# Kernel tuning notes

Hardware: AMD Instinct MI355X
Metric: run time of the kernel (lower is better)

## Reference

```python
import jax, jax.numpy as jnp
import numpy as np

B, D_IN, D_HID, D_OUT = 16384, 256, 512, 256
E, K = 8, 2  # expert_num, activate_num


def setup_inputs() -> dict:
    key = jax.random.key(0)
    ks = jax.random.split(key, 6)
    s_in = 1.0 / np.sqrt(D_IN)
    s_hid = 1.0 / np.sqrt(D_HID)
    return {
        "x": jax.random.normal(ks[0], (B, D_IN), dtype=jnp.float32),
        "Wg": jax.random.normal(ks[1], (D_IN, E), dtype=jnp.float32) * s_in,
        "W1": jax.random.normal(ks[2], (E, D_IN, D_HID), dtype=jnp.float32) * s_in,
        "b1": jnp.zeros((E, D_HID), dtype=jnp.float32),
        "W2": jax.random.normal(ks[3], (E, D_HID, D_OUT), dtype=jnp.float32) * s_hid,
        "b2": jnp.zeros((E, D_OUT), dtype=jnp.float32),
    }


def reference(x, Wg, W1, b1, W2, b2):
    # Gating: logits -> top-k -> softmax over the k selected logits.
    # (nn.Dropout on gate logits is identity at inference.)
    gate_logits = x @ Wg                              # [B, E]
    weights, selected = jax.lax.top_k(gate_logits, K)  # [B, K], [B, K]
    weights = jax.nn.softmax(weights.astype(jnp.float32), axis=1).astype(x.dtype)

    # Expert compute, vectorized over experts (same math as the per-expert
    # gather/compute/scatter loop; tokens not routed to expert e get weight 0).
    h = jax.nn.relu(jnp.einsum("bd,edh->ebh", x, W1) + b1[:, None, :])  # [E, B, H]
    expert_out = jnp.einsum("ebh,eho->ebo", h, W2) + b2[:, None, :]      # [E, B, O]

    # Combine weights: combine[b, e] = sum_k weights[b,k] * [selected[b,k]==e]
    one_hot = jax.nn.one_hot(selected, E, dtype=x.dtype)  # [B, K, E]
    combine = jnp.einsum("bk,bke->be", weights, one_hot)  # [B, E]
    results = jnp.einsum("be,ebo->bo", combine, expert_out)  # [B, O]
    return results
```

## Files before the change

kernel.cpp:

```cpp
#include <hip/hip_runtime.h>
#include <hip/hip_bf16.h>

typedef __bf16 bf16x8 __attribute__((ext_vector_type(8)));
typedef __bf16 bf16x4 __attribute__((ext_vector_type(4)));
typedef float f32x4 __attribute__((ext_vector_type(4)));
typedef float f32x16 __attribute__((ext_vector_type(16)));

#define NTOK 16384
#define DIN  256
#define DHID 512
#define DOUT 256
#define NEXP 8
#define MAXB 264

#define MFMA32(a, b, c) __builtin_amdgcn_mfma_f32_32x32x16_bf16(a, b, c, 0, 0, 0)
#define GLD16(gp, lp)                                                       \
  __builtin_amdgcn_global_load_lds(                                         \
      (__attribute__((address_space(1))) void*)(gp),                        \
      (__attribute__((address_space(3))) void*)(lp), 16, 0, 0)

__global__ __launch_bounds__(256) void prep_kernel(
    const float* __restrict__ x, const float* __restrict__ wg,
    const float* __restrict__ w1, const float* __restrict__ w2,
    int* __restrict__ cnt, int* __restrict__ btok, float* __restrict__ bw,
    __bf16* __restrict__ xbf, __bf16* __restrict__ w1bf,
    __bf16* __restrict__ w2bf) {
  __shared__ int lcnt[NEXP];
  __shared__ int lbase[NEXP];
  const int b = blockIdx.x;
  const int tid = threadIdx.x;

  if (b >= 512) {
    if (b < 1024) {
      int e = (b - 512) >> 6;
      int flat = ((b - 512) & 63) * 256 + tid;
      int kg = flat >> 9;
      int n = flat & 511;
      const float* s = w1 + ((size_t)e * 256 + (size_t)kg * 8) * 512 + n;
      bf16x8 t;
#pragma unroll
      for (int j = 0; j < 8; ++j) t[j] = (__bf16)s[(size_t)j * 512];
      *(bf16x8*)(w1bf + (size_t)(e * 512 + n) * 256 + kg * 8) = t;
    } else {
      int e = (b - 1024) >> 6;
      int fi = ((b - 1024) & 63) * 256 + tid;
      int lane = fi & 63;
      int kw = (fi >> 6) & 3;
      int wo = (fi >> 8) & 7;
      int hc = (fi >> 11) & 7;
      int hid0 = hc * 64 + kw * 16 + (lane >> 5) * 8;
      int o = wo * 32 + (lane & 31);
      const float* s = w2 + ((size_t)e * 512 + hid0) * 256 + o;
      bf16x8 t;
#pragma unroll
      for (int j = 0; j < 8; ++j) t[j] = (__bf16)s[(size_t)j * 256];
      *(bf16x8*)(w2bf + (size_t)e * 131072 + (size_t)fi * 8) = t;
    }
    return;
  }

  if (tid < NEXP) lcnt[tid] = 0;

  const int sub = tid & 7;
  const int tslot = tid >> 3;
  const int token = b * 32 + tslot;
  const f32x4* xr = (const f32x4*)(x + (size_t)token * DIN + sub * 32);
  const float* wr0 = wg + (size_t)sub * 32 * NEXP;

  bf16x8 xb[4];
  f32x4 p0 = {0.f, 0.f, 0.f, 0.f}, p1 = {0.f, 0.f, 0.f, 0.f};
#pragma unroll
  for (int j4 = 0; j4 < 8; ++j4) {
    f32x4 xv = xr[j4];
    const float* wr = wr0 + j4 * 32;
#pragma unroll
    for (int d = 0; d < 4; ++d) {
      float xs_ = xv[d];
      p0 += xs_ * *(const f32x4*)(wr + 8 * d);
      p1 += xs_ * *(const f32x4*)(wr + 8 * d + 4);
      xb[j4 >> 1][(j4 & 1) * 4 + d] = (__bf16)xs_;
    }
  }
  {
    bf16x8* xdst = (bf16x8*)(xbf + (size_t)token * DIN + sub * 32);
#pragma unroll
    for (int i = 0; i < 4; ++i) xdst[i] = xb[i];
  }

  double acc[NEXP];
#pragma unroll
  for (int d = 0; d < 4; ++d) {
    acc[d] = (double)p0[d];
    acc[4 + d] = (double)p1[d];
  }
#pragma unroll
  for (int off = 1; off < 8; off <<= 1)
#pragma unroll
    for (int e = 0; e < NEXP; ++e) acc[e] += __shfl_xor(acc[e], off, 64);

  __syncthreads();

  int i1 = 0, i2 = 0, o1 = 0, o2 = 0;
  float w1s = 0.f, w2s = 0.f;
  if (sub == 0) {
    double bv1 = acc[0];
#pragma unroll
    for (int e = 1; e < NEXP; ++e)
      if (acc[e] > bv1) { bv1 = acc[e]; i1 = e; }
    double bv2 = -1e300;
#pragma unroll
    for (int e = 0; e < NEXP; ++e)
      if (e != i1 && acc[e] > bv2) { bv2 = acc[e]; i2 = e; }
    float dd = expf((float)(bv2 - bv1));
    w1s = 1.0f / (1.0f + dd);
    w2s = dd * w1s;
    o1 = atomicAdd(&lcnt[i1], 1);
    o2 = atomicAdd(&lcnt[i2], 1);
  }
  __syncthreads();
  if (tid < NEXP) lbase[tid] = atomicAdd(&cnt[tid], lcnt[tid]);
  __syncthreads();
  if (sub == 0) {
    int s1 = lbase[i1] + o1, s2 = lbase[i2] + o2;
    btok[i1 * NTOK + s1] = token;
    bw[i1 * NTOK + s1] = w1s;
    btok[i2 * NTOK + s2] = token | 16384;
    bw[i2 * NTOK + s2] = w2s;
  }
}

__global__ __launch_bounds__(512, 2) void ffn_kernel(
    const __bf16* __restrict__ xbf, const __bf16* __restrict__ w1bf,
    const __bf16* __restrict__ w2bf, const float* __restrict__ b1g,
    const float* __restrict__ b2g, const int* __restrict__ cnt,
    const int* __restrict__ btok, const float* __restrict__ bw,
    __bf16* __restrict__ pout) {
  __shared__ __align__(16) __bf16 wb1[2][64 * 256];
  __shared__ __align__(16) __bf16 hs[128 * 64];
  __shared__ int tok[128];
  __shared__ int srow[128];
  __shared__ float wgt[128];
  __shared__ float b1s[DHID];
  __shared__ float b2s[DOUT];

  int b = blockIdx.x;
  int e = -1, start = 0;
  {
    int a0 = 0;
#pragma unroll
    for (int q = 0; q < NEXP; ++q) {
      int t = (cnt[q] + 127) >> 7;
      if (e < 0 && b < a0 + t) { e = q; start = (b - a0) * 128; }
      a0 += t;
    }
  }
  if (e < 0) return;
  const int ce = cnt[e];
  const int rot = (blockIdx.x >> 3) & 7;

  const int tid = threadIdx.x;
  if (tid < 128) {
    int idx = start + tid;
    bool v = idx < ce;
    int entry = v ? btok[e * NTOK + idx] : 0;
    int tk = entry & 16383;
    tok[tid] = tk;
    srow[tid] = (entry >> 14) * NTOK + tk;
    wgt[tid] = v ? bw[e * NTOK + idx] : 0.0f;
  }
  if (tid < 256) b2s[tid] = b2g[e * DOUT + tid];
  b1s[tid & 511] = b1g[e * DHID + (tid & 511)];
  __syncthreads();

  const int lane = tid & 63;
  const int wid = tid >> 6;
  const int hi = lane >> 5;
  const int l31 = lane & 31;
  const int wh = wid >> 2;
  const int wtq = wid & 3;

  bf16x8 xB[16];
  {
    const __bf16* xr = xbf + (size_t)tok[wtq * 32 + l31] * DIN + hi * 8;
#pragma unroll
    for (int kw = 0; kw < 16; ++kw) xB[kw] = *(const bf16x8*)(xr + kw * 16);
  }

  const __bf16* w1e = w1bf + (size_t)e * DHID * DIN;
  const __bf16* w2e = w2bf + (size_t)e * 131072;

  f32x16 acc[4];
#pragma unroll
  for (int bi = 0; bi < 4; ++bi)
#pragma unroll
    for (int r = 0; r < 16; ++r) acc[bi][r] = 0.f;

#define STAGE_W1(bufidx, hcv)                                               \
  {                                                                         \
    _Pragma("unroll")                                                       \
    for (int j = 0; j < 4; ++j) {                                           \
      int W = wid * 4 + j;                                                  \
      int n1 = 2 * W + hi;                                                  \
      int s1 = l31 ^ (n1 & 31);                                             \
      GLD16(w1e + (size_t)((hcv) * 64 + n1) * DIN + s1 * 8,                 \
            &wb1[bufidx][W * 512]);                                         \
    }                                                                       \
  }
#define LOAD_W2(slot, hcv)                                                  \
  {                                                                         \
    const __bf16* w2t = w2e + (size_t)(((hcv) * 8 + wid) * 4) * 512;        \
    _Pragma("unroll")                                                       \
    for (int kw = 0; kw < 4; ++kw)                                          \
      wfrP[slot][kw] = *(const bf16x8*)(w2t + kw * 512 + lane * 8);         \
  }

  bf16x8 wfrP[2][4];
  STAGE_W1(0, rot);
  LOAD_W2(0, rot);

#pragma unroll
  for (int hc0 = 0; hc0 < 8; ++hc0) {
    const int hc = (hc0 + rot) & 7;
    const int cur = hc0 & 1;

    if (hc0 < 7) {
      const int hcn = (hc0 + 1 + rot) & 7;
      STAGE_W1(cur ^ 1, hcn);
      LOAD_W2(cur ^ 1, hcn);
      asm volatile("s_waitcnt vmcnt(8)" ::: "memory");
    } else {
      asm volatile("s_waitcnt vmcnt(0)" ::: "memory");
    }
    __builtin_amdgcn_sched_barrier(0);
    __builtin_amdgcn_s_barrier();
    __builtin_amdgcn_sched_barrier(0);

    f32x16 Sp[2];
#pragma unroll
    for (int r = 0; r < 16; ++r) { Sp[0][r] = 0.f; Sp[1][r] = 0.f; }
#pragma unroll
    for (int kw = 0; kw < 16; ++kw) {
      int row = wh * 32 + l31;
      int s = (kw * 2 + hi) ^ (row & 31);
      bf16x8 a = *(const bf16x8*)((const char*)&wb1[cur][0] + row * 512 + s * 16);
      Sp[kw & 1] = MFMA32(a, xB[kw], Sp[kw & 1]);
    }
    f32x16 S = Sp[0] + Sp[1];
#pragma unroll
    for (int g = 0; g < 4; ++g) {
      int hl = wh * 32 + 8 * g + 4 * hi;
      f32x4 bv = *(const f32x4*)(&b1s[hc * 64 + hl]);
      bf16x4 pk;
#pragma unroll
      for (int r = 0; r < 4; ++r)
        pk[r] = (__bf16)fmaxf(S[4 * g + r] + bv[r], 0.f);
      int m = wtq * 32 + l31;
      int slt = (hl >> 3) ^ (m & 7);
      *(bf16x4*)((char*)hs + m * 128 + slt * 16 + (hl & 7) * 2) = pk;
    }
    asm volatile("s_waitcnt lgkmcnt(0)" ::: "memory");
    __builtin_amdgcn_sched_barrier(0);
    __builtin_amdgcn_s_barrier();
    __builtin_amdgcn_sched_barrier(0);

#pragma unroll
    for (int kw = 0; kw < 4; ++kw) {
#pragma unroll
      for (int bi = 0; bi < 4; ++bi) {
        int m = bi * 32 + l31;
        int s = (kw * 2 + hi) ^ (m & 7);
        bf16x8 hf = *(const bf16x8*)((const char*)hs + m * 128 + s * 16);
        acc[bi] = MFMA32(wfrP[cur][kw], hf, acc[bi]);
      }
    }
  }
#undef STAGE_W1
#undef LOAD_W2

#pragma unroll
  for (int bi = 0; bi < 4; ++bi) {
    int tm = bi * 32 + l31;
    if (start + tm < ce) {
      float wv = wgt[tm];
      __bf16* prow = pout + (size_t)srow[tm] * DOUT;
#pragma unroll
      for (int g = 0; g < 4; ++g) {
        int o0 = wid * 32 + 8 * g + 4 * hi;
        f32x4 bv = *(const f32x4*)(&b2s[o0]);
        bf16x4 pk;
#pragma unroll
        for (int r = 0; r < 4; ++r)
          pk[r] = (__bf16)(wv * (acc[bi][4 * g + r] + bv[r]));
        *(bf16x4*)(prow + o0) = pk;
      }
    }
  }
}

__global__ __launch_bounds__(256) void combine_kernel(const __bf16* __restrict__ pout,
                                                      float* __restrict__ out) {
  int f = blockIdx.x * 256 + threadIdx.x;
  bf16x8 a = *(const bf16x8*)(pout + (size_t)f * 8);
  bf16x8 b = *(const bf16x8*)(pout + (size_t)NTOK * DOUT + (size_t)f * 8);
  float4 o0, o1;
  o0.x = (float)a[0] + (float)b[0];
  o0.y = (float)a[1] + (float)b[1];
  o0.z = (float)a[2] + (float)b[2];
  o0.w = (float)a[3] + (float)b[3];
  o1.x = (float)a[4] + (float)b[4];
  o1.y = (float)a[5] + (float)b[5];
  o1.z = (float)a[6] + (float)b[6];
  o1.w = (float)a[7] + (float)b[7];
  float4* dst = (float4*)(out + (size_t)f * 8);
  dst[0] = o0;
  dst[1] = o1;
}

extern "C" void kernel_launch(void* const* d_in, const int* in_sizes, int n_in,
                              void* d_out, int out_size, void* d_ws, size_t ws_size,
                              hipStream_t stream) {
  const float* x = (const float*)d_in[0];
  const float* Wg = (const float*)d_in[1];
  const float* W1 = (const float*)d_in[2];
  const float* b1 = (const float*)d_in[3];
  const float* W2 = (const float*)d_in[4];
  const float* b2 = (const float*)d_in[5];
  float* out = (float*)d_out;

  char* ws = (char*)d_ws;
  int* cnt = (int*)(ws + 0);
  int* btok = (int*)(ws + 256);
  float* bw = (float*)(ws + 524544);
  __bf16* xbf = (__bf16*)(ws + 1048832);
  __bf16* w1bf = (__bf16*)(ws + 9437440);
  __bf16* w2bf = (__bf16*)(ws + 11534592);
  __bf16* pout = (__bf16*)(ws + 13631744);

  hipMemsetAsync(cnt, 0, NEXP * sizeof(int), stream);

  prep_kernel<<<dim3(1536), dim3(256), 0, stream>>>(x, Wg, W1, W2, cnt, btok,
                                                    bw, xbf, w1bf, w2bf);
  ffn_kernel<<<dim3(MAXB), dim3(512), 0, stream>>>(xbf, w1bf, w2bf, b1, b2,
                                                   cnt, btok, bw, pout);
  combine_kernel<<<dim3(NTOK * DOUT / 8 / 256), dim3(256), 0, stream>>>(pout, out);
}
```

Before: 157.2 us.

## Restructure FFN into independent per-wave 32-token tiles reading weights from global

The FFN kernel drops block-wide LDS staging of W1 and the shared hidden tile. Each wave now owns 32 tokens and half of the output columns, and reads pre-swizzled W1/W2 MFMA fragments straight from global memory. Prep writes W1 in an MFMA-fragment layout to match. This removes the block barriers and LDS staging in exchange for less weight reuse per load. Each output-half wave recomputes the full hidden layer, so first-layer work doubles, and every wave fetches the weights redundantly from L2.

```diff
diff --git a/kernel.cpp b/kernel.cpp
--- a/kernel.cpp
+++ b/kernel.cpp
@@ -11,13 +11,9 @@
 #define DHID 512
 #define DOUT 256
 #define NEXP 8
-#define MAXB 264
+#define MAXB 516
 
 #define MFMA32(a, b, c) __builtin_amdgcn_mfma_f32_32x32x16_bf16(a, b, c, 0, 0, 0)
-#define GLD16(gp, lp)                                                       \
-  __builtin_amdgcn_global_load_lds(                                         \
-      (__attribute__((address_space(1))) void*)(gp),                        \
-      (__attribute__((address_space(3))) void*)(lp), 16, 0, 0)
 
 __global__ __launch_bounds__(256) void prep_kernel(
     const float* __restrict__ x, const float* __restrict__ wg,
@@ -33,23 +29,28 @@
   if (b >= 512) {
     if (b < 1024) {
       int e = (b - 512) >> 6;
-      int flat = ((b - 512) & 63) * 256 + tid;
-      int kg = flat >> 9;
-      int n = flat & 511;
-      const float* s = w1 + ((size_t)e * 256 + (size_t)kg * 8) * 512 + n;
+      int fi = ((b - 512) & 63) * 256 + tid;
+      int lane = fi & 63;
+      int kw = (fi >> 6) & 15;
+      int rt = (fi >> 10) & 1;
+      int hc = (fi >> 11) & 7;
+      int k0 = kw * 16 + (lane >> 5) * 8;
+      int hid = hc * 64 + rt * 32 + (lane & 31);
+      const float* s = w1 + ((size_t)e * 256 + k0) * 512 + hid;
       bf16x8 t;
 #pragma unroll
       for (int j = 0; j < 8; ++j) t[j] = (__bf16)s[(size_t)j * 512];
-      *(bf16x8*)(w1bf + (size_t)(e * 512 + n) * 256 + kg * 8) = t;
+      *(bf16x8*)(w1bf + (size_t)e * 131072 + (size_t)fi * 8) = t;
     } else {
       int e = (b - 1024) >> 6;
       int fi = ((b - 1024) & 63) * 256 + tid;
       int lane = fi & 63;
       int kw = (fi >> 6) & 3;
-      int wo = (fi >> 8) & 7;
+      int ot = (fi >> 8) & 3;
+      int oh = (fi >> 10) & 1;
       int hc = (fi >> 11) & 7;
       int hid0 = hc * 64 + kw * 16 + (lane >> 5) * 8;
-      int o = wo * 32 + (lane & 31);
+      int o = oh * 128 + ot * 32 + (lane & 31);
       const float* s = w2 + ((size_t)e * 512 + hid0) * 256 + o;
       bf16x8 t;
 #pragma unroll
@@ -129,168 +130,121 @@
   }
 }
 
-__global__ __launch_bounds__(512, 2) void ffn_kernel(
+__global__ __launch_bounds__(256, 2) void ffn_kernel(
     const __bf16* __restrict__ xbf, const __bf16* __restrict__ w1bf,
     const __bf16* __restrict__ w2bf, const float* __restrict__ b1g,
     const float* __restrict__ b2g, const int* __restrict__ cnt,
     const int* __restrict__ btok, const float* __restrict__ bw,
     __bf16* __restrict__ pout) {
-  __shared__ __align__(16) __bf16 wb1[2][64 * 256];
-  __shared__ __align__(16) __bf16 hs[128 * 64];
-  __shared__ int tok[128];
-  __shared__ int srow[128];
-  __shared__ float wgt[128];
-  __shared__ float b1s[DHID];
-  __shared__ float b2s[DOUT];
-
-  int b = blockIdx.x;
+  __shared__ __align__(16) __bf16 hscr[4][2][32 * 64];
+
+  const int tid = threadIdx.x;
+  const int lane = tid & 63;
+  const int wid = tid >> 6;
+  const int l31 = lane & 31;
+  const int hi = lane >> 5;
+
+  const int W = blockIdx.x * 4 + wid;
+  const int T = W >> 1;
+  const int oh = W & 1;
+
   int e = -1, start = 0;
   {
     int a0 = 0;
 #pragma unroll
     for (int q = 0; q < NEXP; ++q) {
-      int t = (cnt[q] + 127) >> 7;
-      if (e < 0 && b < a0 + t) { e = q; start = (b - a0) * 128; }
+      int t = (cnt[q] + 31) >> 5;
+      if (e < 0 && T < a0 + t) { e = q; start = (T - a0) * 32; }
       a0 += t;
     }
   }
   if (e < 0) return;
   const int ce = cnt[e];
-  const int rot = (blockIdx.x >> 3) & 7;
-
-  const int tid = threadIdx.x;
-  if (tid < 128) {
-    int idx = start + tid;
-    bool v = idx < ce;
-    int entry = v ? btok[e * NTOK + idx] : 0;
-    int tk = entry & 16383;
-    tok[tid] = tk;
-    srow[tid] = (entry >> 14) * NTOK + tk;
-    wgt[tid] = v ? bw[e * NTOK + idx] : 0.0f;
-  }
-  if (tid < 256) b2s[tid] = b2g[e * DOUT + tid];
-  b1s[tid & 511] = b1g[e * DHID + (tid & 511)];
-  __syncthreads();
-
-  const int lane = tid & 63;
-  const int wid = tid >> 6;
-  const int hi = lane >> 5;
-  const int l31 = lane & 31;
-  const int wh = wid >> 2;
-  const int wtq = wid & 3;
+
+  const int idx = start + l31;
+  const bool v = idx < ce;
+  const int entry = v ? btok[e * NTOK + idx] : 0;
+  const int mytok = entry & 16383;
+  const int msrow = (entry >> 14) * NTOK + mytok;
+  const float mwgt = v ? bw[e * NTOK + idx] : 0.0f;
 
   bf16x8 xB[16];
   {
-    const __bf16* xr = xbf + (size_t)tok[wtq * 32 + l31] * DIN + hi * 8;
+    const __bf16* xr = xbf + (size_t)mytok * DIN + hi * 8;
 #pragma unroll
     for (int kw = 0; kw < 16; ++kw) xB[kw] = *(const bf16x8*)(xr + kw * 16);
   }
 
-  const __bf16* w1e = w1bf + (size_t)e * DHID * DIN;
+  const __bf16* w1e = w1bf + (size_t)e * 131072;
   const __bf16* w2e = w2bf + (size_t)e * 131072;
+  const float* b1e = b1g + e * DHID;
+  const float* b2e = b2g + e * DOUT;
 
   f32x16 acc[4];
 #pragma unroll
-  for (int bi = 0; bi < 4; ++bi)
-#pragma unroll
-    for (int r = 0; r < 16; ++r) acc[bi][r] = 0.f;
-
-#define STAGE_W1(bufidx, hcv)                                               \
-  {                                                                         \
-    _Pragma("unroll")                                                       \
-    for (int j = 0; j < 4; ++j) {                                           \
-      int W = wid * 4 + j;                                                  \
-      int n1 = 2 * W + hi;                                                  \
-      int s1 = l31 ^ (n1 & 31);                                             \
-      GLD16(w1e + (size_t)((hcv) * 64 + n1) * DIN + s1 * 8,                 \
-            &wb1[bufidx][W * 512]);                                         \
-    }                                                                       \
-  }
-#define LOAD_W2(slot, hcv)                                                  \
-  {                                                                         \
-    const __bf16* w2t = w2e + (size_t)(((hcv) * 8 + wid) * 4) * 512;        \
-    _Pragma("unroll")                                                       \
-    for (int kw = 0; kw < 4; ++kw)                                          \
-      wfrP[slot][kw] = *(const bf16x8*)(w2t + kw * 512 + lane * 8);         \
-  }
-
-  bf16x8 wfrP[2][4];
-  STAGE_W1(0, rot);
-  LOAD_W2(0, rot);
+  for (int ot = 0; ot < 4; ++ot)
+#pragma unroll
+    for (int r = 0; r < 16; ++r) acc[ot][r] = 0.f;
+
+  const int rot = (W >> 3) & 7;
 
 #pragma unroll
   for (int hc0 = 0; hc0 < 8; ++hc0) {
     const int hc = (hc0 + rot) & 7;
-    const int cur = hc0 & 1;
-
-    if (hc0 < 7) {
-      const int hcn = (hc0 + 1 + rot) & 7;
-      STAGE_W1(cur ^ 1, hcn);
-      LOAD_W2(cur ^ 1, hcn);
-      asm volatile("s_waitcnt vmcnt(8)" ::: "memory");
-    } else {
-      asm volatile("s_waitcnt vmcnt(0)" ::: "memory");
-    }
-    __builtin_amdgcn_sched_barrier(0);
-    __builtin_amdgcn_s_barrier();
-    __builtin_amdgcn_sched_barrier(0);
-
-    f32x16 Sp[2];
-#pragma unroll
-    for (int r = 0; r < 16; ++r) { Sp[0][r] = 0.f; Sp[1][r] = 0.f; }
-#pragma unroll
-    for (int kw = 0; kw < 16; ++kw) {
-      int row = wh * 32 + l31;
-      int s = (kw * 2 + hi) ^ (row & 31);
-      bf16x8 a = *(const bf16x8*)((const char*)&wb1[cur][0] + row * 512 + s * 16);
-      Sp[kw & 1] = MFMA32(a, xB[kw], Sp[kw & 1]);
-    }
-    f32x16 S = Sp[0] + Sp[1];
-#pragma unroll
-    for (int g = 0; g < 4; ++g) {
-      int hl = wh * 32 + 8 * g + 4 * hi;
-      f32x4 bv = *(const f32x4*)(&b1s[hc * 64 + hl]);
-      bf16x4 pk;
-#pragma unroll
-      for (int r = 0; r < 4; ++r)
-        pk[r] = (__bf16)fmaxf(S[4 * g + r] + bv[r], 0.f);
-      int m = wtq * 32 + l31;
-      int slt = (hl >> 3) ^ (m & 7);
-      *(bf16x4*)((char*)hs + m * 128 + slt * 16 + (hl & 7) * 2) = pk;
+    __bf16* hb = &hscr[wid][hc0 & 1][0];
+
+    const __bf16* w1c = w1e + (size_t)hc * 16384;
+#pragma unroll
+    for (int rt = 0; rt < 2; ++rt) {
+      f32x16 Sp[2];
+#pragma unroll
+      for (int r = 0; r < 16; ++r) { Sp[0][r] = 0.f; Sp[1][r] = 0.f; }
+#pragma unroll
+      for (int kw = 0; kw < 16; ++kw) {
+        bf16x8 a = *(const bf16x8*)(w1c + (size_t)((rt * 16 + kw) * 64 + lane) * 8);
+        Sp[kw & 1] = MFMA32(a, xB[kw], Sp[kw & 1]);
+      }
+      f32x16 S = Sp[0] + Sp[1];
+#pragma unroll
+      for (int g = 0; g < 4; ++g) {
+        int hl = rt * 32 + 8 * g + 4 * hi;
+        f32x4 bv = *(const f32x4*)(b1e + hc * 64 + hl);
+        bf16x4 pk;
+#pragma unroll
+        for (int r = 0; r < 4; ++r)
+          pk[r] = (__bf16)fmaxf(S[4 * g + r] + bv[r], 0.f);
+        int slt = (hl >> 3) ^ (l31 & 7);
+        *(bf16x4*)((char*)hb + l31 * 128 + slt * 16 + (hl & 7) * 2) = pk;
+      }
     }
     asm volatile("s_waitcnt lgkmcnt(0)" ::: "memory");
     __builtin_amdgcn_sched_barrier(0);
-    __builtin_amdgcn_s_barrier();
-    __builtin_amdgcn_sched_barrier(0);
-
+
+    const __bf16* w2c = w2e + (size_t)hc * 16384 + (size_t)oh * 8192;
 #pragma unroll
     for (int kw = 0; kw < 4; ++kw) {
-#pragma unroll
-      for (int bi = 0; bi < 4; ++bi) {
-        int m = bi * 32 + l31;
-        int s = (kw * 2 + hi) ^ (m & 7);
-        bf16x8 hf = *(const bf16x8*)((const char*)hs + m * 128 + s * 16);
-        acc[bi] = MFMA32(wfrP[cur][kw], hf, acc[bi]);
+      int s = (kw * 2 + hi) ^ (l31 & 7);
+      bf16x8 hf = *(const bf16x8*)((const char*)hb + l31 * 128 + s * 16);
+#pragma unroll
+      for (int ot = 0; ot < 4; ++ot) {
+        bf16x8 wf = *(const bf16x8*)(w2c + (size_t)((ot * 4 + kw) * 64 + lane) * 8);
+        acc[ot] = MFMA32(wf, hf, acc[ot]);
       }
     }
   }
-#undef STAGE_W1
-#undef LOAD_W2
-
-#pragma unroll
-  for (int bi = 0; bi < 4; ++bi) {
-    int tm = bi * 32 + l31;
-    if (start + tm < ce) {
-      float wv = wgt[tm];
-      __bf16* prow = pout + (size_t)srow[tm] * DOUT;
+
+  if (v) {
+    __bf16* prow = pout + (size_t)msrow * DOUT;
+#pragma unroll
+    for (int ot = 0; ot < 4; ++ot) {
 #pragma unroll
       for (int g = 0; g < 4; ++g) {
-        int o0 = wid * 32 + 8 * g + 4 * hi;
-        f32x4 bv = *(const f32x4*)(&b2s[o0]);
+        int o0 = oh * 128 + ot * 32 + 8 * g + 4 * hi;
+        f32x4 bv = *(const f32x4*)(b2e + o0);
         bf16x4 pk;
 #pragma unroll
         for (int r = 0; r < 4; ++r)
-          pk[r] = (__bf16)(wv * (acc[bi][4 * g + r] + bv[r]));
+          pk[r] = (__bf16)(mwgt * (acc[ot][4 * g + r] + bv[r]));
         *(bf16x4*)(prow + o0) = pk;
       }
     }
@@ -340,7 +294,7 @@
 
   prep_kernel<<<dim3(1536), dim3(256), 0, stream>>>(x, Wg, W1, W2, cnt, btok,
                                                     bw, xbf, w1bf, w2bf);
-  ffn_kernel<<<dim3(MAXB), dim3(512), 0, stream>>>(xbf, w1bf, w2bf, b1, b2,
+  ffn_kernel<<<dim3(MAXB), dim3(256), 0, stream>>>(xbf, w1bf, w2bf, b1, b2,
                                                    cnt, btok, bw, pout);
   combine_kernel<<<dim3(NTOK * DOUT / 8 / 256), dim3(256), 0, stream>>>(pout, out);
 }
```

New measurement: 267.1 us. 1.7x slower.

## Fuse prep, FFN and combine into one persistent cooperative kernel

Applied to the files above, without the earlier changes.

Merges the three launches (routing/convert, expert FFN, combine) into a single cooperative kernel of 256 blocks with grid-wide syncs between phases. The FFN phase becomes a persistent loop pulling full 128-token tiles from an atomic ticket counter. Remainder tokens go through a second ticket loop of 32-token per-wave units that read weights straight from global memory. This removes launch gaps and tail imbalance, at the cost of two grid barriers and less occupancy, since there is one block per CU and no 2-block launch bound.

```diff
diff --git a/kernel.cpp b/kernel.cpp
--- a/kernel.cpp
+++ b/kernel.cpp
@@ -1,5 +1,8 @@
 #include <hip/hip_runtime.h>
+#include <hip/hip_cooperative_groups.h>
 #include <hip/hip_bf16.h>
+
+namespace cg = cooperative_groups;
 
 typedef __bf16 bf16x8 __attribute__((ext_vector_type(8)));
 typedef __bf16 bf16x4 __attribute__((ext_vector_type(4)));
@@ -11,7 +14,6 @@
 #define DHID 512
 #define DOUT 256
 #define NEXP 8
-#define MAXB 264
 
 #define MFMA32(a, b, c) __builtin_amdgcn_mfma_f32_32x32x16_bf16(a, b, c, 0, 0, 0)
 #define GLD16(gp, lp)                                                       \
@@ -19,122 +21,14 @@
       (__attribute__((address_space(1))) void*)(gp),                        \
       (__attribute__((address_space(3))) void*)(lp), 16, 0, 0)
 
-__global__ __launch_bounds__(256) void prep_kernel(
+__global__ __launch_bounds__(512) void moe_kernel(
     const float* __restrict__ x, const float* __restrict__ wg,
-    const float* __restrict__ w1, const float* __restrict__ w2,
+    const float* __restrict__ w1, const float* __restrict__ b1g,
+    const float* __restrict__ w2, const float* __restrict__ b2g,
     int* __restrict__ cnt, int* __restrict__ btok, float* __restrict__ bw,
     __bf16* __restrict__ xbf, __bf16* __restrict__ w1bf,
-    __bf16* __restrict__ w2bf) {
-  __shared__ int lcnt[NEXP];
-  __shared__ int lbase[NEXP];
-  const int b = blockIdx.x;
-  const int tid = threadIdx.x;
-
-  if (b >= 512) {
-    if (b < 1024) {
-      int e = (b - 512) >> 6;
-      int flat = ((b - 512) & 63) * 256 + tid;
-      int kg = flat >> 9;
-      int n = flat & 511;
-      const float* s = w1 + ((size_t)e * 256 + (size_t)kg * 8) * 512 + n;
-      bf16x8 t;
-#pragma unroll
-      for (int j = 0; j < 8; ++j) t[j] = (__bf16)s[(size_t)j * 512];
-      *(bf16x8*)(w1bf + (size_t)(e * 512 + n) * 256 + kg * 8) = t;
-    } else {
-      int e = (b - 1024) >> 6;
-      int fi = ((b - 1024) & 63) * 256 + tid;
-      int lane = fi & 63;
-      int kw = (fi >> 6) & 3;
-      int wo = (fi >> 8) & 7;
-      int hc = (fi >> 11) & 7;
-      int hid0 = hc * 64 + kw * 16 + (lane >> 5) * 8;
-      int o = wo * 32 + (lane & 31);
-      const float* s = w2 + ((size_t)e * 512 + hid0) * 256 + o;
-      bf16x8 t;
-#pragma unroll
-      for (int j = 0; j < 8; ++j) t[j] = (__bf16)s[(size_t)j * 256];
-      *(bf16x8*)(w2bf + (size_t)e * 131072 + (size_t)fi * 8) = t;
-    }
-    return;
-  }
-
-  if (tid < NEXP) lcnt[tid] = 0;
-
-  const int sub = tid & 7;
-  const int tslot = tid >> 3;
-  const int token = b * 32 + tslot;
-  const f32x4* xr = (const f32x4*)(x + (size_t)token * DIN + sub * 32);
-  const float* wr0 = wg + (size_t)sub * 32 * NEXP;
-
-  bf16x8 xb[4];
-  f32x4 p0 = {0.f, 0.f, 0.f, 0.f}, p1 = {0.f, 0.f, 0.f, 0.f};
-#pragma unroll
-  for (int j4 = 0; j4 < 8; ++j4) {
-    f32x4 xv = xr[j4];
-    const float* wr = wr0 + j4 * 32;
-#pragma unroll
-    for (int d = 0; d < 4; ++d) {
-      float xs_ = xv[d];
-      p0 += xs_ * *(const f32x4*)(wr + 8 * d);
-      p1 += xs_ * *(const f32x4*)(wr + 8 * d + 4);
-      xb[j4 >> 1][(j4 & 1) * 4 + d] = (__bf16)xs_;
-    }
-  }
-  {
-    bf16x8* xdst = (bf16x8*)(xbf + (size_t)token * DIN + sub * 32);
-#pragma unroll
-    for (int i = 0; i < 4; ++i) xdst[i] = xb[i];
-  }
-
-  double acc[NEXP];
-#pragma unroll
-  for (int d = 0; d < 4; ++d) {
-    acc[d] = (double)p0[d];
-    acc[4 + d] = (double)p1[d];
-  }
-#pragma unroll
-  for (int off = 1; off < 8; off <<= 1)
-#pragma unroll
-    for (int e = 0; e < NEXP; ++e) acc[e] += __shfl_xor(acc[e], off, 64);
-
-  __syncthreads();
-
-  int i1 = 0, i2 = 0, o1 = 0, o2 = 0;
-  float w1s = 0.f, w2s = 0.f;
-  if (sub == 0) {
-    double bv1 = acc[0];
-#pragma unroll
-    for (int e = 1; e < NEXP; ++e)
-      if (acc[e] > bv1) { bv1 = acc[e]; i1 = e; }
-    double bv2 = -1e300;
-#pragma unroll
-    for (int e = 0; e < NEXP; ++e)
-      if (e != i1 && acc[e] > bv2) { bv2 = acc[e]; i2 = e; }
-    float dd = expf((float)(bv2 - bv1));
-    w1s = 1.0f / (1.0f + dd);
-    w2s = dd * w1s;
-    o1 = atomicAdd(&lcnt[i1], 1);
-    o2 = atomicAdd(&lcnt[i2], 1);
-  }
-  __syncthreads();
-  if (tid < NEXP) lbase[tid] = atomicAdd(&cnt[tid], lcnt[tid]);
-  __syncthreads();
-  if (sub == 0) {
-    int s1 = lbase[i1] + o1, s2 = lbase[i2] + o2;
-    btok[i1 * NTOK + s1] = token;
-    bw[i1 * NTOK + s1] = w1s;
-    btok[i2 * NTOK + s2] = token | 16384;
-    bw[i2 * NTOK + s2] = w2s;
-  }
-}
-
-__global__ __launch_bounds__(512, 2) void ffn_kernel(
-    const __bf16* __restrict__ xbf, const __bf16* __restrict__ w1bf,
-    const __bf16* __restrict__ w2bf, const float* __restrict__ b1g,
-    const float* __restrict__ b2g, const int* __restrict__ cnt,
-    const int* __restrict__ btok, const float* __restrict__ bw,
-    __bf16* __restrict__ pout) {
+    __bf16* __restrict__ w2bf, __bf16* __restrict__ pout,
+    float* __restrict__ out) {
   __shared__ __align__(16) __bf16 wb1[2][64 * 256];
   __shared__ __align__(16) __bf16 hs[128 * 64];
   __shared__ int tok[128];
@@ -142,58 +36,178 @@
   __shared__ float wgt[128];
   __shared__ float b1s[DHID];
   __shared__ float b2s[DOUT];
-
-  int b = blockIdx.x;
-  int e = -1, start = 0;
-  {
-    int a0 = 0;
-#pragma unroll
-    for (int q = 0; q < NEXP; ++q) {
-      int t = (cnt[q] + 127) >> 7;
-      if (e < 0 && b < a0 + t) { e = q; start = (b - a0) * 128; }
-      a0 += t;
-    }
-  }
-  if (e < 0) return;
-  const int ce = cnt[e];
-  const int rot = (blockIdx.x >> 3) & 7;
-
+  __shared__ int lcnt[NEXP];
+  __shared__ int lbase[NEXP];
+  __shared__ int tk_s;
+
+  const int b = blockIdx.x;
   const int tid = threadIdx.x;
-  if (tid < 128) {
-    int idx = start + tid;
-    bool v = idx < ce;
-    int entry = v ? btok[e * NTOK + idx] : 0;
-    int tk = entry & 16383;
-    tok[tid] = tk;
-    srow[tid] = (entry >> 14) * NTOK + tk;
-    wgt[tid] = v ? bw[e * NTOK + idx] : 0.0f;
-  }
-  if (tid < 256) b2s[tid] = b2g[e * DOUT + tid];
-  b1s[tid & 511] = b1g[e * DHID + (tid & 511)];
-  __syncthreads();
-
   const int lane = tid & 63;
   const int wid = tid >> 6;
   const int hi = lane >> 5;
   const int l31 = lane & 31;
-  const int wh = wid >> 2;
-  const int wtq = wid & 3;
-
-  bf16x8 xB[16];
+
   {
-    const __bf16* xr = xbf + (size_t)tok[wtq * 32 + l31] * DIN + hi * 8;
-#pragma unroll
-    for (int kw = 0; kw < 16; ++kw) xB[kw] = *(const bf16x8*)(xr + kw * 16);
-  }
-
-  const __bf16* w1e = w1bf + (size_t)e * DHID * DIN;
-  const __bf16* w2e = w2bf + (size_t)e * 131072;
-
-  f32x16 acc[4];
-#pragma unroll
-  for (int bi = 0; bi < 4; ++bi)
-#pragma unroll
-    for (int r = 0; r < 16; ++r) acc[bi][r] = 0.f;
+    if (tid < NEXP) lcnt[tid] = 0;
+    const int sub = tid & 7;
+    const int tslot = tid >> 3;
+    const int token = b * 64 + tslot;
+    const f32x4* xr = (const f32x4*)(x + (size_t)token * DIN + sub * 32);
+    const float* wr0 = wg + (size_t)sub * 32 * NEXP;
+
+    bf16x8 xb[4];
+    f32x4 p0 = {0.f, 0.f, 0.f, 0.f}, p1 = {0.f, 0.f, 0.f, 0.f};
+#pragma unroll
+    for (int j4 = 0; j4 < 8; ++j4) {
+      f32x4 xv = xr[j4];
+      const float* wr = wr0 + j4 * 32;
+#pragma unroll
+      for (int d = 0; d < 4; ++d) {
+        float xs_ = xv[d];
+        p0 += xs_ * *(const f32x4*)(wr + 8 * d);
+        p1 += xs_ * *(const f32x4*)(wr + 8 * d + 4);
+        xb[j4 >> 1][(j4 & 1) * 4 + d] = (__bf16)xs_;
+      }
+    }
+    {
+      bf16x8* xdst = (bf16x8*)(xbf + (size_t)token * DIN + sub * 32);
+#pragma unroll
+      for (int i = 0; i < 4; ++i) xdst[i] = xb[i];
+    }
+
+    double acc[NEXP];
+#pragma unroll
+    for (int d = 0; d < 4; ++d) {
+      acc[d] = (double)p0[d];
+      acc[4 + d] = (double)p1[d];
+    }
+#pragma unroll
+    for (int off = 1; off < 8; off <<= 1)
+#pragma unroll
+      for (int e = 0; e < NEXP; ++e) acc[e] += __shfl_xor(acc[e], off, 64);
+
+    __syncthreads();
+
+    int i1 = 0, i2 = 0, o1 = 0, o2 = 0;
+    float w1s = 0.f, w2s = 0.f;
+    if (sub == 0) {
+      double bv1 = acc[0];
+#pragma unroll
+      for (int e = 1; e < NEXP; ++e)
+        if (acc[e] > bv1) { bv1 = acc[e]; i1 = e; }
+      double bv2 = -1e300;
+#pragma unroll
+      for (int e = 0; e < NEXP; ++e)
+        if (e != i1 && acc[e] > bv2) { bv2 = acc[e]; i2 = e; }
+      float dd = expf((float)(bv2 - bv1));
+      w1s = 1.0f / (1.0f + dd);
+      w2s = dd * w1s;
+      o1 = atomicAdd(&lcnt[i1], 1);
+      o2 = atomicAdd(&lcnt[i2], 1);
+    }
+    __syncthreads();
+    if (tid < NEXP) lbase[tid] = atomicAdd(&cnt[tid], lcnt[tid]);
+    __syncthreads();
+    if (sub == 0) {
+      int s1 = lbase[i1] + o1, s2 = lbase[i2] + o2;
+      btok[i1 * NTOK + s1] = token;
+      bw[i1 * NTOK + s1] = w1s;
+      btok[i2 * NTOK + s2] = token | 16384;
+      bw[i2 * NTOK + s2] = w2s;
+    }
+  }
+
+  {
+    int u = b * 512 + tid;
+    int e = u >> 14;
+    int flat = u & 16383;
+    {
+      int kg = flat >> 9;
+      int n = flat & 511;
+      const float* s = w1 + ((size_t)e * 256 + (size_t)kg * 8) * 512 + n;
+      bf16x8 t;
+#pragma unroll
+      for (int j = 0; j < 8; ++j) t[j] = (__bf16)s[(size_t)j * 512];
+      *(bf16x8*)(w1bf + (size_t)(e * 512 + n) * 256 + kg * 8) = t;
+    }
+    {
+      int lane2 = flat & 63;
+      int kw = (flat >> 6) & 3;
+      int wo = (flat >> 8) & 7;
+      int hc = (flat >> 11) & 7;
+      int hid0 = hc * 64 + kw * 16 + (lane2 >> 5) * 8;
+      int o = wo * 32 + (lane2 & 31);
+      const float* s = w2 + ((size_t)e * 512 + hid0) * 256 + o;
+      bf16x8 t;
+#pragma unroll
+      for (int j = 0; j < 8; ++j) t[j] = (__bf16)s[(size_t)j * 256];
+      *(bf16x8*)(w2bf + (size_t)e * 131072 + (size_t)flat * 8) = t;
+    }
+  }
+
+  __threadfence();
+  cg::this_grid().sync();
+  __threadfence();
+
+  int cn_[NEXP], nb_[NEXP], Bp[NEXP + 1], Up[NEXP + 1];
+  Bp[0] = 0; Up[0] = 0;
+#pragma unroll
+  for (int q = 0; q < NEXP; ++q) {
+    cn_[q] = cnt[q];
+    nb_[q] = cn_[q] >> 7;
+    Bp[q + 1] = Bp[q] + nb_[q];
+    int rm = cn_[q] - (nb_[q] << 7);
+    Up[q + 1] = Up[q] + ((rm + 31) >> 5);
+  }
+  const int nbig = Bp[NEXP];
+  const int nun = Up[NEXP];
+  const int ntt = (nun + 3) >> 2;
+  int* tick = cnt + 8;
+  int* ttick = cnt + 9;
+  const int rot = (b >> 3) & 7;
+
+  for (;;) {
+    __syncthreads();
+    if (tid == 0) tk_s = atomicAdd(tick, 1);
+    __syncthreads();
+    const int t = tk_s;
+    if (t >= nbig) break;
+    int e = -1, start = 0, ce = 0;
+#pragma unroll
+    for (int q = 0; q < NEXP; ++q)
+      if (e < 0 && t < Bp[q + 1]) { e = q; start = (t - Bp[q]) * 128; ce = cn_[q]; }
+
+    if (tid < 128) {
+      int idx = start + tid;
+      bool v = idx < ce;
+      int entry = v ? btok[e * NTOK + idx] : 0;
+      int tk = entry & 16383;
+      tok[tid] = tk;
+      srow[tid] = (entry >> 14) * NTOK + tk;
+      wgt[tid] = v ? bw[e * NTOK + idx] : 0.0f;
+    }
+    if (tid < 256) b2s[tid] = b2g[e * DOUT + tid];
+    b1s[tid & 511] = b1g[e * DHID + (tid & 511)];
+    __syncthreads();
+
+    const int wh = wid >> 2;
+    const int wtq = wid & 3;
+
+    bf16x8 xB[16];
+    {
+      const __bf16* xr2 = xbf + (size_t)tok[wtq * 32 + l31] * DIN + hi * 8;
+#pragma unroll
+      for (int kw = 0; kw < 16; ++kw) xB[kw] = *(const bf16x8*)(xr2 + kw * 16);
+    }
+
+    const __bf16* w1e = w1bf + (size_t)e * DHID * DIN;
+    const __bf16* w2e = w2bf + (size_t)e * 131072;
+
+    f32x16 acc[4];
+#pragma unroll
+    for (int bi = 0; bi < 4; ++bi)
+#pragma unroll
+      for (int r = 0; r < 16; ++r) acc[bi][r] = 0.f;
 
 #define STAGE_W1(bufidx, hcv)                                               \
   {                                                                         \
@@ -214,106 +228,213 @@
       wfrP[slot][kw] = *(const bf16x8*)(w2t + kw * 512 + lane * 8);         \
   }
 
-  bf16x8 wfrP[2][4];
-  STAGE_W1(0, rot);
-  LOAD_W2(0, rot);
-
-#pragma unroll
-  for (int hc0 = 0; hc0 < 8; ++hc0) {
-    const int hc = (hc0 + rot) & 7;
-    const int cur = hc0 & 1;
-
-    if (hc0 < 7) {
-      const int hcn = (hc0 + 1 + rot) & 7;
-      STAGE_W1(cur ^ 1, hcn);
-      LOAD_W2(cur ^ 1, hcn);
-      asm volatile("s_waitcnt vmcnt(8)" ::: "memory");
-    } else {
-      asm volatile("s_waitcnt vmcnt(0)" ::: "memory");
-    }
-    __builtin_amdgcn_sched_barrier(0);
-    __builtin_amdgcn_s_barrier();
-    __builtin_amdgcn_sched_barrier(0);
-
-    f32x16 Sp[2];
-#pragma unroll
-    for (int r = 0; r < 16; ++r) { Sp[0][r] = 0.f; Sp[1][r] = 0.f; }
-#pragma unroll
-    for (int kw = 0; kw < 16; ++kw) {
-      int row = wh * 32 + l31;
-      int s = (kw * 2 + hi) ^ (row & 31);
-      bf16x8 a = *(const bf16x8*)((const char*)&wb1[cur][0] + row * 512 + s * 16);
-      Sp[kw & 1] = MFMA32(a, xB[kw], Sp[kw & 1]);
-    }
-    f32x16 S = Sp[0] + Sp[1];
-#pragma unroll
-    for (int g = 0; g < 4; ++g) {
-      int hl = wh * 32 + 8 * g + 4 * hi;
-      f32x4 bv = *(const f32x4*)(&b1s[hc * 64 + hl]);
-      bf16x4 pk;
-#pragma unroll
-      for (int r = 0; r < 4; ++r)
-        pk[r] = (__bf16)fmaxf(S[4 * g + r] + bv[r], 0.f);
-      int m = wtq * 32 + l31;
-      int slt = (hl >> 3) ^ (m & 7);
-      *(bf16x4*)((char*)hs + m * 128 + slt * 16 + (hl & 7) * 2) = pk;
-    }
-    asm volatile("s_waitcnt lgkmcnt(0)" ::: "memory");
-    __builtin_amdgcn_sched_barrier(0);
-    __builtin_amdgcn_s_barrier();
-    __builtin_amdgcn_sched_barrier(0);
-
-#pragma unroll
-    for (int kw = 0; kw < 4; ++kw) {
-#pragma unroll
-      for (int bi = 0; bi < 4; ++bi) {
-        int m = bi * 32 + l31;
-        int s = (kw * 2 + hi) ^ (m & 7);
-        bf16x8 hf = *(const bf16x8*)((const char*)hs + m * 128 + s * 16);
-        acc[bi] = MFMA32(wfrP[cur][kw], hf, acc[bi]);
-      }
-    }
-  }
+    bf16x8 wfrP[2][4];
+    STAGE_W1(0, rot);
+    LOAD_W2(0, rot);
+
+#pragma unroll
+    for (int hc0 = 0; hc0 < 8; ++hc0) {
+      const int hc = (hc0 + rot) & 7;
+      const int cur = hc0 & 1;
+
+      if (hc0 < 7) {
+        const int hcn = (hc0 + 1 + rot) & 7;
+        STAGE_W1(cur ^ 1, hcn);
+        LOAD_W2(cur ^ 1, hcn);
+        asm volatile("s_waitcnt vmcnt(8)" ::: "memory");
+      } else {
+        asm volatile("s_waitcnt vmcnt(0)" ::: "memory");
+      }
+      __builtin_amdgcn_sched_barrier(0);
+      __builtin_amdgcn_s_barrier();
+      __builtin_amdgcn_sched_barrier(0);
+
+      f32x16 Sp[2];
+#pragma unroll
+      for (int r = 0; r < 16; ++r) { Sp[0][r] = 0.f; Sp[1][r] = 0.f; }
+#pragma unroll
+      for (int kw = 0; kw < 16; ++kw) {
+        int row = wh * 32 + l31;
+        int s = (kw * 2 + hi) ^ (row & 31);
+        bf16x8 a = *(const bf16x8*)((const char*)&wb1[cur][0] + row * 512 + s * 16);
+        Sp[kw & 1] = MFMA32(a, xB[kw], Sp[kw & 1]);
+      }
+      f32x16 S = Sp[0] + Sp[1];
+#pragma unroll
+      for (int g = 0; g < 4; ++g) {
+        int hl = wh * 32 + 8 * g + 4 * hi;
+        f32x4 bv = *(const f32x4*)(&b1s[hc * 64 + hl]);
+        bf16x4 pk;
+#pragma unroll
+        for (int r = 0; r < 4; ++r)
+          pk[r] = (__bf16)fmaxf(S[4 * g + r] + bv[r], 0.f);
+        int m = wtq * 32 + l31;
+        int slt = (hl >> 3) ^ (m & 7);
+        *(bf16x4*)((char*)hs + m * 128 + slt * 16 + (hl & 7) * 2) = pk;
+      }
+      asm volatile("s_waitcnt lgkmcnt(0)" ::: "memory");
+      __builtin_amdgcn_sched_barrier(0);
+      __builtin_amdgcn_s_barrier();
+      __builtin_amdgcn_sched_barrier(0);
+
+#pragma unroll
+      for (int kw = 0; kw < 4; ++kw) {
+#pragma unroll
+        for (int bi = 0; bi < 4; ++bi) {
+          int m = bi * 32 + l31;
+          int s = (kw * 2 + hi) ^ (m & 7);
+          bf16x8 hf = *(const bf16x8*)((const char*)hs + m * 128 + s * 16);
+          acc[bi] = MFMA32(wfrP[cur][kw], hf, acc[bi]);
+        }
+      }
+    }
 #undef STAGE_W1
 #undef LOAD_W2
 
 #pragma unroll
-  for (int bi = 0; bi < 4; ++bi) {
-    int tm = bi * 32 + l31;
-    if (start + tm < ce) {
-      float wv = wgt[tm];
-      __bf16* prow = pout + (size_t)srow[tm] * DOUT;
-#pragma unroll
-      for (int g = 0; g < 4; ++g) {
-        int o0 = wid * 32 + 8 * g + 4 * hi;
-        f32x4 bv = *(const f32x4*)(&b2s[o0]);
-        bf16x4 pk;
-#pragma unroll
-        for (int r = 0; r < 4; ++r)
-          pk[r] = (__bf16)(wv * (acc[bi][4 * g + r] + bv[r]));
-        *(bf16x4*)(prow + o0) = pk;
-      }
-    }
-  }
-}
-
-__global__ __launch_bounds__(256) void combine_kernel(const __bf16* __restrict__ pout,
-                                                      float* __restrict__ out) {
-  int f = blockIdx.x * 256 + threadIdx.x;
-  bf16x8 a = *(const bf16x8*)(pout + (size_t)f * 8);
-  bf16x8 b = *(const bf16x8*)(pout + (size_t)NTOK * DOUT + (size_t)f * 8);
-  float4 o0, o1;
-  o0.x = (float)a[0] + (float)b[0];
-  o0.y = (float)a[1] + (float)b[1];
-  o0.z = (float)a[2] + (float)b[2];
-  o0.w = (float)a[3] + (float)b[3];
-  o1.x = (float)a[4] + (float)b[4];
-  o1.y = (float)a[5] + (float)b[5];
-  o1.z = (float)a[6] + (float)b[6];
-  o1.w = (float)a[7] + (float)b[7];
-  float4* dst = (float4*)(out + (size_t)f * 8);
-  dst[0] = o0;
-  dst[1] = o1;
+    for (int bi = 0; bi < 4; ++bi) {
+      int tm = bi * 32 + l31;
+      if (start + tm < ce) {
+        float wv = wgt[tm];
+        __bf16* prow = pout + (size_t)srow[tm] * DOUT;
+#pragma unroll
+        for (int g = 0; g < 4; ++g) {
+          int o0 = wid * 32 + 8 * g + 4 * hi;
+          f32x4 bv = *(const f32x4*)(&b2s[o0]);
+          bf16x4 pk;
+#pragma unroll
+          for (int r = 0; r < 4; ++r)
+            pk[r] = (__bf16)(wv * (acc[bi][4 * g + r] + bv[r]));
+          *(bf16x4*)(prow + o0) = pk;
+        }
+      }
+    }
+  }
+
+  for (;;) {
+    __syncthreads();
+    if (tid == 0) tk_s = atomicAdd(ttick, 1);
+    __syncthreads();
+    const int tt = tk_s;
+    if (tt >= ntt) break;
+    const int unit = tt * 4 + (wid >> 1);
+    if (unit < nun) {
+      int e = -1, k = 0, nbv = 0, ce = 0;
+#pragma unroll
+      for (int q = 0; q < NEXP; ++q)
+        if (e < 0 && unit < Up[q + 1]) { e = q; k = unit - Up[q]; nbv = nb_[q]; ce = cn_[q]; }
+      const int start = (nbv << 7) + k * 32;
+      const int oh = wid & 1;
+      __bf16* hb = (__bf16*)((char*)&wb1[0][0] + wid * 4096);
+
+      const int idx = start + l31;
+      const bool v = idx < ce;
+      const int entry = v ? btok[e * NTOK + idx] : 0;
+      const int mytok = entry & 16383;
+      const int msrow = (entry >> 14) * NTOK + mytok;
+      const float mwgt = v ? bw[e * NTOK + idx] : 0.0f;
+
+      bf16x8 xB2[16];
+      {
+        const __bf16* xr2 = xbf + (size_t)mytok * DIN + hi * 8;
+#pragma unroll
+        for (int kw = 0; kw < 16; ++kw) xB2[kw] = *(const bf16x8*)(xr2 + kw * 16);
+      }
+      const __bf16* w1r = w1bf + (size_t)e * DHID * DIN;
+      const __bf16* w2t = w2bf + (size_t)e * 131072;
+      const float* b1e = b1g + e * DHID;
+      const float* b2e = b2g + e * DOUT;
+
+      f32x16 ac[4];
+#pragma unroll
+      for (int ot = 0; ot < 4; ++ot)
+#pragma unroll
+        for (int r = 0; r < 16; ++r) ac[ot][r] = 0.f;
+
+#pragma unroll
+      for (int hc = 0; hc < 8; ++hc) {
+        asm volatile("s_waitcnt lgkmcnt(0)" ::: "memory");
+        __builtin_amdgcn_sched_barrier(0);
+#pragma unroll
+        for (int rt = 0; rt < 2; ++rt) {
+          f32x16 Sp[2];
+#pragma unroll
+          for (int r = 0; r < 16; ++r) { Sp[0][r] = 0.f; Sp[1][r] = 0.f; }
+#pragma unroll
+          for (int kw = 0; kw < 16; ++kw) {
+            bf16x8 a = *(const bf16x8*)(w1r +
+                (size_t)(hc * 64 + rt * 32 + l31) * 256 + kw * 16 + hi * 8);
+            Sp[kw & 1] = MFMA32(a, xB2[kw], Sp[kw & 1]);
+          }
+          f32x16 S = Sp[0] + Sp[1];
+#pragma unroll
+          for (int g = 0; g < 4; ++g) {
+            int hl = rt * 32 + 8 * g + 4 * hi;
+            f32x4 bv = *(const f32x4*)(b1e + hc * 64 + hl);
+            bf16x4 pk;
+#pragma unroll
+            for (int r = 0; r < 4; ++r)
+              pk[r] = (__bf16)fmaxf(S[4 * g + r] + bv[r], 0.f);
+            int slt = (hl >> 3) ^ (l31 & 7);
+            *(bf16x4*)((char*)hb + l31 * 128 + slt * 16 + (hl & 7) * 2) = pk;
+          }
+        }
+        asm volatile("s_waitcnt lgkmcnt(0)" ::: "memory");
+        __builtin_amdgcn_sched_barrier(0);
+#pragma unroll
+        for (int kw = 0; kw < 4; ++kw) {
+          int s = (kw * 2 + hi) ^ (l31 & 7);
+          bf16x8 hf = *(const bf16x8*)((const char*)hb + l31 * 128 + s * 16);
+#pragma unroll
+          for (int ot = 0; ot < 4; ++ot) {
+            bf16x8 wf = *(const bf16x8*)(w2t +
+                (size_t)(((hc * 8 + (oh * 4 + ot)) * 4 + kw) * 512) + lane * 8);
+            ac[ot] = MFMA32(wf, hf, ac[ot]);
+          }
+        }
+      }
+
+      if (v) {
+        __bf16* prow = pout + (size_t)msrow * DOUT;
+#pragma unroll
+        for (int ot = 0; ot < 4; ++ot) {
+#pragma unroll
+          for (int g = 0; g < 4; ++g) {
+            int o0 = oh * 128 + ot * 32 + 8 * g + 4 * hi;
+            f32x4 bv = *(const f32x4*)(b2e + o0);
+            bf16x4 pk;
+#pragma unroll
+            for (int r = 0; r < 4; ++r)
+              pk[r] = (__bf16)(mwgt * (ac[ot][4 * g + r] + bv[r]));
+            *(bf16x4*)(prow + o0) = pk;
+          }
+        }
+      }
+    }
+  }
+
+  __threadfence();
+  cg::this_grid().sync();
+  __threadfence();
+
+#pragma unroll
+  for (int i = 0; i < 4; ++i) {
+    int f = i * 131072 + b * 512 + tid;
+    bf16x8 a = *(const bf16x8*)(pout + (size_t)f * 8);
+    bf16x8 bb = *(const bf16x8*)(pout + (size_t)NTOK * DOUT + (size_t)f * 8);
+    float4 o0, o1;
+    o0.x = (float)a[0] + (float)bb[0];
+    o0.y = (float)a[1] + (float)bb[1];
+    o0.z = (float)a[2] + (float)bb[2];
+    o0.w = (float)a[3] + (float)bb[3];
+    o1.x = (float)a[4] + (float)bb[4];
+    o1.y = (float)a[5] + (float)bb[5];
+    o1.z = (float)a[6] + (float)bb[6];
+    o1.w = (float)a[7] + (float)bb[7];
+    float4* dst = (float4*)(out + (size_t)f * 8);
+    dst[0] = o0;
+    dst[1] = o1;
+  }
 }
 
 extern "C" void kernel_launch(void* const* d_in, const int* in_sizes, int n_in,
@@ -336,11 +457,12 @@
   __bf16* w2bf = (__bf16*)(ws + 11534592);
   __bf16* pout = (__bf16*)(ws + 13631744);
 
-  hipMemsetAsync(cnt, 0, NEXP * sizeof(int), stream);
-
-  prep_kernel<<<dim3(1536), dim3(256), 0, stream>>>(x, Wg, W1, W2, cnt, btok,
-                                                    bw, xbf, w1bf, w2bf);
-  ffn_kernel<<<dim3(MAXB), dim3(512), 0, stream>>>(xbf, w1bf, w2bf, b1, b2,
-                                                   cnt, btok, bw, pout);
-  combine_kernel<<<dim3(NTOK * DOUT / 8 / 256), dim3(256), 0, stream>>>(pout, out);
+  hipMemsetAsync(cnt, 0, 64, stream);
+
+  void* kargs[] = {(void*)&x,    (void*)&Wg,   (void*)&W1,  (void*)&b1,
+                   (void*)&W2,   (void*)&b2,   (void*)&cnt, (void*)&btok,
+                   (void*)&bw,   (void*)&xbf,  (void*)&w1bf, (void*)&w2bf,
+                   (void*)&pout, (void*)&out};
+  hipLaunchCooperativeKernel((const void*)moe_kernel, dim3(256), dim3(512),
+                             kargs, 0, stream);
 }
```

After: 477.9 us. +204.0%, slower.

## Software-pipeline FFN chunks by double-buffering hidden tile across iterations

Applied to the files above, without the earlier changes.

Double-buffers the hidden-activation LDS tile so the second GEMM for chunk i-1 runs in the same phase as the first GEMM for chunk i. This removes one barrier-separated phase per iteration and lets the two MFMA streams interleave. The W2 fragment load moves to the current iteration and the last chunk's second GEMM is drained after the loop. LDS use grows by 16KB per block, which with launch bounds of 2 blocks may limit occupancy. The vmcnt(8) wait now also has to cover the W2 register loads issued just before it.

```diff
diff --git a/kernel.cpp b/kernel.cpp
--- a/kernel.cpp
+++ b/kernel.cpp
@@ -136,7 +136,7 @@
     const int* __restrict__ btok, const float* __restrict__ bw,
     __bf16* __restrict__ pout) {
   __shared__ __align__(16) __bf16 wb1[2][64 * 256];
-  __shared__ __align__(16) __bf16 hs[128 * 64];
+  __shared__ __align__(16) __bf16 hs[2][128 * 64];
   __shared__ int tok[128];
   __shared__ int srow[128];
   __shared__ float wgt[128];
@@ -216,62 +216,74 @@
 
   bf16x8 wfrP[2][4];
   STAGE_W1(0, rot);
-  LOAD_W2(0, rot);
-
-#pragma unroll
-  for (int hc0 = 0; hc0 < 8; ++hc0) {
-    const int hc = (hc0 + rot) & 7;
-    const int cur = hc0 & 1;
-
-    if (hc0 < 7) {
-      const int hcn = (hc0 + 1 + rot) & 7;
-      STAGE_W1(cur ^ 1, hcn);
-      LOAD_W2(cur ^ 1, hcn);
-      asm volatile("s_waitcnt vmcnt(8)" ::: "memory");
-    } else {
-      asm volatile("s_waitcnt vmcnt(0)" ::: "memory");
-    }
+
+#pragma unroll
+  for (int i = 0; i < 8; ++i) {
+    const int cur = i & 1;
+    const int hc = (i + rot) & 7;
+
+    if (i < 7) STAGE_W1(cur ^ 1, (i + 1 + rot) & 7);
+    LOAD_W2(cur, hc);
+    __builtin_amdgcn_sched_barrier(0);
+    asm volatile("s_waitcnt vmcnt(8)" ::: "memory");
     __builtin_amdgcn_sched_barrier(0);
     __builtin_amdgcn_s_barrier();
     __builtin_amdgcn_sched_barrier(0);
 
-    f32x16 Sp[2];
-#pragma unroll
-    for (int r = 0; r < 16; ++r) { Sp[0][r] = 0.f; Sp[1][r] = 0.f; }
-#pragma unroll
-    for (int kw = 0; kw < 16; ++kw) {
-      int row = wh * 32 + l31;
-      int s = (kw * 2 + hi) ^ (row & 31);
-      bf16x8 a = *(const bf16x8*)((const char*)&wb1[cur][0] + row * 512 + s * 16);
-      Sp[kw & 1] = MFMA32(a, xB[kw], Sp[kw & 1]);
-    }
-    f32x16 S = Sp[0] + Sp[1];
-#pragma unroll
-    for (int g = 0; g < 4; ++g) {
-      int hl = wh * 32 + 8 * g + 4 * hi;
-      f32x4 bv = *(const f32x4*)(&b1s[hc * 64 + hl]);
-      bf16x4 pk;
-#pragma unroll
-      for (int r = 0; r < 4; ++r)
-        pk[r] = (__bf16)fmaxf(S[4 * g + r] + bv[r], 0.f);
-      int m = wtq * 32 + l31;
-      int slt = (hl >> 3) ^ (m & 7);
-      *(bf16x4*)((char*)hs + m * 128 + slt * 16 + (hl & 7) * 2) = pk;
+    if (i > 0) {
+#pragma unroll
+      for (int kw = 0; kw < 4; ++kw) {
+#pragma unroll
+        for (int bi = 0; bi < 4; ++bi) {
+          int m = bi * 32 + l31;
+          int s = (kw * 2 + hi) ^ (m & 7);
+          bf16x8 hf =
+              *(const bf16x8*)((const char*)&hs[cur ^ 1][0] + m * 128 + s * 16);
+          acc[bi] = MFMA32(wfrP[cur ^ 1][kw], hf, acc[bi]);
+        }
+      }
+    }
+
+    {
+      f32x16 Sp[2];
+#pragma unroll
+      for (int r = 0; r < 16; ++r) { Sp[0][r] = 0.f; Sp[1][r] = 0.f; }
+#pragma unroll
+      for (int kw = 0; kw < 16; ++kw) {
+        int row = wh * 32 + l31;
+        int s = (kw * 2 + hi) ^ (row & 31);
+        bf16x8 a =
+            *(const bf16x8*)((const char*)&wb1[cur][0] + row * 512 + s * 16);
+        Sp[kw & 1] = MFMA32(a, xB[kw], Sp[kw & 1]);
+      }
+      f32x16 S = Sp[0] + Sp[1];
+#pragma unroll
+      for (int g = 0; g < 4; ++g) {
+        int hl = wh * 32 + 8 * g + 4 * hi;
+        f32x4 bv = *(const f32x4*)(&b1s[hc * 64 + hl]);
+        bf16x4 pk;
+#pragma unroll
+        for (int r = 0; r < 4; ++r)
+          pk[r] = (__bf16)fmaxf(S[4 * g + r] + bv[r], 0.f);
+        int m = wtq * 32 + l31;
+        int slt = (hl >> 3) ^ (m & 7);
+        *(bf16x4*)((char*)&hs[cur][0] + m * 128 + slt * 16 + (hl & 7) * 2) = pk;
+      }
     }
     asm volatile("s_waitcnt lgkmcnt(0)" ::: "memory");
     __builtin_amdgcn_sched_barrier(0);
     __builtin_amdgcn_s_barrier();
-    __builtin_amdgcn_sched_barrier(0);
-
-#pragma unroll
-    for (int kw = 0; kw < 4; ++kw) {
-#pragma unroll
-      for (int bi = 0; bi < 4; ++bi) {
-        int m = bi * 32 + l31;
-        int s = (kw * 2 + hi) ^ (m & 7);
-        bf16x8 hf = *(const bf16x8*)((const char*)hs + m * 128 + s * 16);
-        acc[bi] = MFMA32(wfrP[cur][kw], hf, acc[bi]);
-      }
+  }
+
+  asm volatile("s_waitcnt vmcnt(0)" ::: "memory");
+#pragma unroll
+  for (int kw = 0; kw < 4; ++kw) {
+#pragma unroll
+    for (int bi = 0; bi < 4; ++bi) {
+      int m = bi * 32 + l31;
+      int s = (kw * 2 + hi) ^ (m & 7);
+      bf16x8 hf = *(const bf16x8*)((const char*)&hs[1][0] + m * 128 + s * 16);
+      acc[bi] = MFMA32(wfrP[1][kw], hf, acc[bi]);
     }
   }
 #undef STAGE_W1
```

After: 157.6 us. No clear change (+0.2%).
